# Kernel tuning notes

Hardware: AMD Instinct MI355X
Metric: run time of the kernel (lower is better)

The kernel has to match this reference:

```python
import jax, jax.numpy as jnp
import numpy as np

H = 16   # num_heads
K = 2    # top_k experts per token


def _layer_norm(x, g, b, eps=1e-5):
    mu = jnp.mean(x, axis=-1, keepdims=True)
    var = jnp.mean(jnp.square(x - mu), axis=-1, keepdims=True)
    return (x - mu) * jax.lax.rsqrt(var + eps) * g + b


def setup_inputs() -> dict:
    key = jax.random.key(0)
    ks = jax.random.split(key, 8)
    B, S, D, E = 2, 2048, 1024, 8
    sc = 0.02
    return {
        "x": jax.random.normal(ks[0], (B, S, D), jnp.float32),
        "wq": jax.random.normal(ks[1], (D, D), jnp.float32) * sc,
        "wk": jax.random.normal(ks[2], (D, D), jnp.float32) * sc,
        "wv": jax.random.normal(ks[3], (D, D), jnp.float32) * sc,
        "wo": jax.random.normal(ks[4], (D, D), jnp.float32) * sc,
        "ln1_g": jnp.ones((D,), jnp.float32),
        "ln1_b": jnp.zeros((D,), jnp.float32),
        "ln2_g": jnp.ones((D,), jnp.float32),
        "ln2_b": jnp.zeros((D,), jnp.float32),
        "router_w": jax.random.normal(ks[5], (E, D), jnp.float32) * sc,
        "expert_w": jax.random.normal(ks[6], (E, D, D), jnp.float32) * sc,
    }


def reference(x, wq, wk, wv, wo, ln1_g, ln1_b, ln2_g, ln2_b, router_w, expert_w):
    B, S, D = x.shape
    E = expert_w.shape[0]
    hd = D // H

    # ---- attention sublayer: x = x + attn(norm1(x)) ----
    h = _layer_norm(x, ln1_g, ln1_b)
    q = (h @ wq.T).reshape(B, S, H, hd).transpose(0, 2, 1, 3)  # bhsd
    k = (h @ wk.T).reshape(B, S, H, hd).transpose(0, 2, 1, 3)
    v = (h @ wv.T).reshape(B, S, H, hd).transpose(0, 2, 1, 3)
    scores = jnp.einsum("bhqd,bhkd->bhqk", q, k) / jnp.sqrt(jnp.float32(hd))
    causal = jnp.tril(jnp.ones((S, S), dtype=bool))
    scores = jnp.where(causal, scores, jnp.finfo(scores.dtype).min)
    probs = jax.nn.softmax(scores, axis=-1)
    attn = jnp.einsum("bhqk,bhkd->bhqd", probs, v)
    attn = attn.transpose(0, 2, 1, 3).reshape(B, S, D) @ wo.T
    x = x + attn

    # ---- MoE sublayer: x = x + moe(norm2(x)) ----
    h2 = _layer_norm(x, ln2_g, ln2_b)
    logits = jnp.einsum("bsd,ed->bse", h2, router_w)          # [B,S,E]
    top_logits, top_ids = jax.lax.top_k(logits, K)            # [B,S,K]
    gates = jax.nn.softmax(top_logits, axis=-1)               # [B,S,K]
    # dense combine weights over experts (E is small): sum_k gate_k * onehot(id_k)
    combine = jnp.sum(jax.nn.one_hot(top_ids, E, dtype=h2.dtype) * gates[..., None], axis=-2)  # [B,S,E]
    # per-token matvec with expert weights: token @ W_e.T for each expert, then weighted sum
    y = jnp.einsum("bsd,eod->bseo", h2, expert_w)             # [B,S,E,D]
    moe_out = jnp.einsum("bse,bseo->bso", combine, y)
    return x + moe_out
```

## Files before the change

### kernel.cpp

```cpp
#include <hip/hip_runtime.h>
#include <hip/hip_bf16.h>
#include <cstdint>


typedef __bf16 bf16;
typedef __bf16 bf16x8 __attribute__((ext_vector_type(8)));
typedef __bf16 bf16x4 __attribute__((ext_vector_type(4)));
typedef float f32x4 __attribute__((ext_vector_type(4)));
typedef float f32x16 __attribute__((ext_vector_type(16)));

#define MFMA(a, b, c) __builtin_amdgcn_mfma_f32_16x16x32_bf16(a, b, c, 0, 0, 0)
#define MFMA32(a, b, c) __builtin_amdgcn_mfma_f32_32x32x16_bf16(a, b, c, 0, 0, 0)

__device__ __forceinline__ void gld16(void* lds, const void* g) {
  __builtin_amdgcn_global_load_lds(
      (const __attribute__((address_space(1))) void*)g,
      (__attribute__((address_space(3))) void*)lds, 16, 0, 0);
}

__global__ void prep_weights(const float* __restrict__ wq, const float* __restrict__ wk,
                             const float* __restrict__ wv, const float* __restrict__ wo,
                             const float* __restrict__ expw,
                             bf16* __restrict__ wqh, bf16* __restrict__ wql,
                             bf16* __restrict__ wkh, bf16* __restrict__ wkl,
                             bf16* __restrict__ wvh, bf16* __restrict__ wvl,
                             bf16* __restrict__ woh, bf16* __restrict__ wol,
                             bf16* __restrict__ ewh) {
  int bid = blockIdx.x;
  if (bid < 4096) {
    int wsel = bid >> 10;
    const float* src = wsel == 0 ? wq : wsel == 1 ? wk : wsel == 2 ? wv : wo;
    bf16* hi = wsel == 0 ? wqh : wsel == 1 ? wkh : wsel == 2 ? wvh : woh;
    bf16* lo = wsel == 0 ? wql : wsel == 1 ? wkl : wsel == 2 ? wvl : wol;
    int i = ((bid & 1023) * 256 + threadIdx.x) * 4;
    float4 v = *(const float4*)(src + i);
    float a[4] = {v.x, v.y, v.z, v.w};
#pragma unroll
    for (int j = 0; j < 4; j++) {
      bf16 h = (bf16)a[j];
      hi[i + j] = h;
      lo[i + j] = (bf16)(a[j] - (float)h);
    }
  } else {
    int i = ((bid - 4096) * 256 + threadIdx.x) * 4;
    float4 v = *(const float4*)(expw + i);
    ewh[i] = (bf16)v.x; ewh[i + 1] = (bf16)v.y;
    ewh[i + 2] = (bf16)v.z; ewh[i + 3] = (bf16)v.w;
  }
}

__global__ void ln_split(const float* __restrict__ x, const float* __restrict__ g,
                         const float* __restrict__ b, bf16* __restrict__ hi,
                         bf16* __restrict__ lo) {
  int tok = blockIdx.x, t = threadIdx.x;
  float4 v = ((const float4*)(x + (size_t)tok * 1024))[t];
  float s = v.x + v.y + v.z + v.w;
  float ss = v.x * v.x + v.y * v.y + v.z * v.z + v.w * v.w;
#pragma unroll
  for (int o = 1; o < 64; o <<= 1) { s += __shfl_xor(s, o); ss += __shfl_xor(ss, o); }
  __shared__ float red[8];
  int w = t >> 6, lane = t & 63;
  if (lane == 0) { red[w] = s; red[4 + w] = ss; }
  __syncthreads();
  s = red[0] + red[1] + red[2] + red[3];
  ss = red[4] + red[5] + red[6] + red[7];
  float mu = s * (1.f / 1024.f);
  float rstd = rsqrtf(ss * (1.f / 1024.f) - mu * mu + 1e-5f);
  float4 gv = ((const float4*)g)[t], bv = ((const float4*)b)[t];
  float y[4] = {(v.x - mu) * rstd * gv.x + bv.x, (v.y - mu) * rstd * gv.y + bv.y,
                (v.z - mu) * rstd * gv.z + bv.z, (v.w - mu) * rstd * gv.w + bv.w};
  size_t o = (size_t)tok * 1024 + t * 4;
#pragma unroll
  for (int j = 0; j < 4; j++) {
    bf16 h = (bf16)y[j];
    hi[o + j] = h;
    lo[o + j] = (bf16)(y[j] - (float)h);
  }
}

__global__ void ln2route(const float* __restrict__ x1, const float* __restrict__ g,
                         const float* __restrict__ b, const float* __restrict__ rw,
                         bf16* __restrict__ h2h, int* __restrict__ eid,
                         float2* __restrict__ gout) {
  int tok = blockIdx.x, t = threadIdx.x;
  float4 v = ((const float4*)(x1 + (size_t)tok * 1024))[t];
  float s = v.x + v.y + v.z + v.w;
  float ss = v.x * v.x + v.y * v.y + v.z * v.z + v.w * v.w;
#pragma unroll
  for (int o = 1; o < 64; o <<= 1) { s += __shfl_xor(s, o); ss += __shfl_xor(ss, o); }
  __shared__ float red[8];
  __shared__ float h2s[1024];
  __shared__ float lg[8];
  int w = t >> 6, lane = t & 63;
  if (lane == 0) { red[w] = s; red[4 + w] = ss; }
  __syncthreads();
  s = red[0] + red[1] + red[2] + red[3];
  ss = red[4] + red[5] + red[6] + red[7];
  float mu = s * (1.f / 1024.f);
  float rstd = rsqrtf(ss * (1.f / 1024.f) - mu * mu + 1e-5f);
  float4 gv = ((const float4*)g)[t], bv = ((const float4*)b)[t];
  float4 y;
  y.x = (v.x - mu) * rstd * gv.x + bv.x;
  y.y = (v.y - mu) * rstd * gv.y + bv.y;
  y.z = (v.z - mu) * rstd * gv.z + bv.z;
  y.w = (v.w - mu) * rstd * gv.w + bv.w;
  ((float4*)h2s)[t] = y;
  size_t o = (size_t)tok * 1024 + t * 4;
  h2h[o] = (bf16)y.x; h2h[o + 1] = (bf16)y.y;
  h2h[o + 2] = (bf16)y.z; h2h[o + 3] = (bf16)y.w;
  __syncthreads();
  float a0 = 0.f, a1 = 0.f;
  const float4* r0 = (const float4*)(rw + (2 * w) * 1024);
  const float4* r1 = (const float4*)(rw + (2 * w + 1) * 1024);
#pragma unroll
  for (int it = 0; it < 4; it++) {
    float4 xv = ((const float4*)h2s)[lane + 64 * it];
    float4 w0 = r0[lane + 64 * it];
    float4 w1 = r1[lane + 64 * it];
    a0 += xv.x * w0.x + xv.y * w0.y + xv.z * w0.z + xv.w * w0.w;
    a1 += xv.x * w1.x + xv.y * w1.y + xv.z * w1.z + xv.w * w1.w;
  }
#pragma unroll
  for (int o2 = 1; o2 < 64; o2 <<= 1) {
    a0 += __shfl_xor(a0, o2);
    a1 += __shfl_xor(a1, o2);
  }
  if (lane == 0) { lg[2 * w] = a0; lg[2 * w + 1] = a1; }
  __syncthreads();
  if (t == 0) {
    int i0 = 0; float l0 = lg[0];
#pragma unroll
    for (int e = 1; e < 8; e++) if (lg[e] > l0) { l0 = lg[e]; i0 = e; }
    int i1 = -1; float l1 = -3e38f;
#pragma unroll
    for (int e = 0; e < 8; e++) if (e != i0 && lg[e] > l1) { l1 = lg[e]; i1 = e; }
    float e1 = __expf(l1 - l0);
    float den = 1.f + e1;
    eid[tok] = i0 | (i1 << 4);
    gout[tok] = make_float2(1.f / den, e1 / den);
  }
}

__global__ void build_lists(const int* __restrict__ eid,
                            const float2* __restrict__ gv,
                            int* __restrict__ tlist, float* __restrict__ glist,
                            int* __restrict__ cnt) {
  int e = blockIdx.x, t = threadIdx.x;
  int lane = t & 63, w = t >> 6;
  __shared__ int wt[4];
  int base = 0;
  for (int c = 0; c < 16; c++) {
    int tok = c * 256 + t;
    int pair = eid[tok];
    int e0 = pair & 15, e1 = pair >> 4;
    bool p = (e0 == e) || (e1 == e);
    float2 g2 = gv[tok];
    float gate = (e0 == e) ? g2.x : g2.y;
    unsigned long long m = __ballot(p);
    int rank = __popcll(m & ((1ull << lane) - 1ull));
    if (lane == 0) wt[w] = __popcll(m);
    __syncthreads();
    int off = base;
    for (int i = 0; i < w; i++) off += wt[i];
    if (p) {
      tlist[e * 4096 + off + rank] = tok;
      glist[e * 4096 + off + rank] = gate;
    }
    base += wt[0] + wt[1] + wt[2] + wt[3];
    __syncthreads();
  }
  if (t == 0) cnt[e] = base;
  int pad = (base + 127) & ~127;
  if (pad > 4096) pad = 4096;
  for (int i = base + t; i < pad; i += 256) {
    tlist[e * 4096 + i] = 0;
    glist[e * 4096 + i] = 0.f;
  }
}

__device__ __forceinline__ void gemm_core_split(
    const bf16* __restrict__ Ah, const bf16* __restrict__ Al,
    const bf16* __restrict__ Bh, const bf16* __restrict__ Bl, int m0, int n0,
    f32x4 (&acc)[4][4]) {
  __shared__ __align__(16) bf16 As_h[4096], As_l[4096], Bs_h[4096], Bs_l[4096];
  int t = threadIdx.x, lane = t & 63, w = t >> 6;
  int i0 = t, i1 = t + 256;
  const bf16* a0h = Ah + (size_t)(m0 + (i0 >> 2)) * 1024 + (i0 & 3) * 8;
  const bf16* a1h = Ah + (size_t)(m0 + (i1 >> 2)) * 1024 + (i1 & 3) * 8;
  const bf16* a0l = Al + (size_t)(m0 + (i0 >> 2)) * 1024 + (i0 & 3) * 8;
  const bf16* a1l = Al + (size_t)(m0 + (i1 >> 2)) * 1024 + (i1 & 3) * 8;
  const bf16* b0h = Bh + (size_t)(n0 + (i0 >> 2)) * 1024 + (i0 & 3) * 8;
  const bf16* b1h = Bh + (size_t)(n0 + (i1 >> 2)) * 1024 + (i1 & 3) * 8;
  const bf16* b0l = Bl + (size_t)(n0 + (i0 >> 2)) * 1024 + (i0 & 3) * 8;
  const bf16* b1l = Bl + (size_t)(n0 + (i1 >> 2)) * 1024 + (i1 & 3) * 8;
  int wm = (w >> 1) * 64, wn = (w & 1) * 64;
  int lr = lane & 15, lq = lane >> 4;
  for (int k0 = 0; k0 < 1024; k0 += 32) {
    __syncthreads();
    gld16(&As_h[i0 * 8], a0h + k0); gld16(&As_h[i1 * 8], a1h + k0);
    gld16(&As_l[i0 * 8], a0l + k0); gld16(&As_l[i1 * 8], a1l + k0);
    gld16(&Bs_h[i0 * 8], b0h + k0); gld16(&Bs_h[i1 * 8], b1h + k0);
    gld16(&Bs_l[i0 * 8], b0l + k0); gld16(&Bs_l[i1 * 8], b1l + k0);
    __syncthreads();
    bf16x8 ah[4], al4[4], bh[4], bl4[4];
#pragma unroll
    for (int i = 0; i < 4; i++) {
      ah[i]  = *(const bf16x8*)&As_h[(wm + i * 16 + lr) * 32 + lq * 8];
      al4[i] = *(const bf16x8*)&As_l[(wm + i * 16 + lr) * 32 + lq * 8];
      bh[i]  = *(const bf16x8*)&Bs_h[(wn + i * 16 + lr) * 32 + lq * 8];
      bl4[i] = *(const bf16x8*)&Bs_l[(wn + i * 16 + lr) * 32 + lq * 8];
    }
#pragma unroll
    for (int i = 0; i < 4; i++)
#pragma unroll
      for (int j = 0; j < 4; j++) {
        f32x4 c = acc[i][j];
        c = MFMA(ah[i], bh[j], c);
        c = MFMA(ah[i], bl4[j], c);
        c = MFMA(al4[i], bh[j], c);
        acc[i][j] = c;
      }
  }
}

__global__ __launch_bounds__(256, 2) void gemm_qk(
    const bf16* __restrict__ hh, const bf16* __restrict__ hl,
    const bf16* __restrict__ wqh, const bf16* __restrict__ wql,
    const bf16* __restrict__ wkh, const bf16* __restrict__ wkl,
    bf16* __restrict__ qh, bf16* __restrict__ ql, bf16* __restrict__ kh,
    bf16* __restrict__ kl) {
  int n0 = blockIdx.x * 128, m0 = blockIdx.y * 128, z = blockIdx.z;
  const bf16* Bh = z ? wkh : wqh;
  const bf16* Bl = z ? wkl : wql;
  f32x4 acc[4][4];
#pragma unroll
  for (int i = 0; i < 4; i++)
#pragma unroll
    for (int j = 0; j < 4; j++) acc[i][j] = (f32x4){0.f, 0.f, 0.f, 0.f};
  gemm_core_split(hh, hl, Bh, Bl, m0, n0, acc);
  int t = threadIdx.x, lane = t & 63, w = t >> 6;
  int wm = (w >> 1) * 64, wn = (w & 1) * 64, lr = lane & 15, lq = lane >> 4;
  bf16* Oh = z ? kh : qh;
  bf16* Ol = z ? kl : ql;
  float scale = z ? 1.0f : (0.125f * 1.44269504f);
#pragma unroll
  for (int i = 0; i < 4; i++)
#pragma unroll
    for (int j = 0; j < 4; j++)
#pragma unroll
      for (int r = 0; r < 4; r++) {
        size_t row = m0 + wm + i * 16 + lq * 4 + r;
        int col = n0 + wn + j * 16 + lr;
        float v = acc[i][j][r] * scale;
        bf16 h = (bf16)v;
        Oh[row * 1024 + col] = h;
        Ol[row * 1024 + col] = (bf16)(v - (float)h);
      }
}

__global__ __launch_bounds__(256, 2) void gemm_v(
    const bf16* __restrict__ A, const bf16* __restrict__ B,
    bf16* __restrict__ vth) {
  int n0 = blockIdx.x * 128, m0 = blockIdx.y * 128;
  __shared__ __align__(16) bf16 As[4096], Bs[4096];
  int t = threadIdx.x, lane = t & 63, w = t >> 6;
  int i0 = t, i1 = t + 256;
  const bf16* a0 = A + (size_t)(m0 + (i0 >> 2)) * 1024 + (i0 & 3) * 8;
  const bf16* a1 = A + (size_t)(m0 + (i1 >> 2)) * 1024 + (i1 & 3) * 8;
  const bf16* b0 = B + (size_t)(n0 + (i0 >> 2)) * 1024 + (i0 & 3) * 8;
  const bf16* b1 = B + (size_t)(n0 + (i1 >> 2)) * 1024 + (i1 & 3) * 8;
  int wm = (w >> 1) * 64, wn = (w & 1) * 64, lr = lane & 15, lq = lane >> 4;
  f32x4 acc[4][4];
#pragma unroll
  for (int i = 0; i < 4; i++)
#pragma unroll
    for (int j = 0; j < 4; j++) acc[i][j] = (f32x4){0.f, 0.f, 0.f, 0.f};
  for (int k0 = 0; k0 < 1024; k0 += 32) {
    __syncthreads();
    gld16(&As[i0 * 8], a0 + k0); gld16(&As[i1 * 8], a1 + k0);
    gld16(&Bs[i0 * 8], b0 + k0); gld16(&Bs[i1 * 8], b1 + k0);
    __syncthreads();
    bf16x8 af[4], bfr[4];
#pragma unroll
    for (int i = 0; i < 4; i++) {
      af[i] = *(const bf16x8*)&As[(wm + i * 16 + lr) * 32 + lq * 8];
      bfr[i] = *(const bf16x8*)&Bs[(wn + i * 16 + lr) * 32 + lq * 8];
    }
#pragma unroll
    for (int i = 0; i < 4; i++)
#pragma unroll
      for (int j = 0; j < 4; j++) acc[i][j] = MFMA(af[i], bfr[j], acc[i][j]);
  }
  int bb = m0 >> 11;
  int srow0 = m0 & 2047;
#pragma unroll
  for (int i = 0; i < 4; i++)
#pragma unroll
    for (int j = 0; j < 4; j++) {
      int col = n0 + wn + j * 16 + lr;
      int head = col >> 6, d = col & 63;
      int s = srow0 + wm + i * 16 + lq * 4;
      int ss = (s & ~63) | (((((s >> 2) & 15)) ^ (d & 15)) << 2);
      bf16x4 hv;
#pragma unroll
      for (int r = 0; r < 4; r++) hv[r] = (bf16)acc[i][j][r];
      size_t off = ((size_t)((bb * 16 + head) * 64 + d)) * 2048 + ss;
      *(bf16x4*)(vth + off) = hv;
    }
}

__global__ __launch_bounds__(256, 2) void gemm_wo(
    const bf16* __restrict__ ah, const bf16* __restrict__ al,
    const bf16* __restrict__ bh, const bf16* __restrict__ bl,
    const float* __restrict__ resid, float* __restrict__ outp) {
  int n0 = blockIdx.x * 128, m0 = blockIdx.y * 128;
  f32x4 acc[4][4];
#pragma unroll
  for (int i = 0; i < 4; i++)
#pragma unroll
    for (int j = 0; j < 4; j++) acc[i][j] = (f32x4){0.f, 0.f, 0.f, 0.f};
  gemm_core_split(ah, al, bh, bl, m0, n0, acc);
  int t = threadIdx.x, lane = t & 63, w = t >> 6;
  int wm = (w >> 1) * 64, wn = (w & 1) * 64, lr = lane & 15, lq = lane >> 4;
#pragma unroll
  for (int i = 0; i < 4; i++)
#pragma unroll
    for (int j = 0; j < 4; j++)
#pragma unroll
      for (int r = 0; r < 4; r++) {
        size_t row = m0 + wm + i * 16 + lq * 4 + r;
        int col = n0 + wn + j * 16 + lr;
        outp[row * 1024 + col] = resid[row * 1024 + col] + acc[i][j][r];
      }
}

__global__ __launch_bounds__(256, 3) void attn_fused(
    const bf16* __restrict__ qh, const bf16* __restrict__ ql,
    const bf16* __restrict__ kh, const bf16* __restrict__ kl,
    const bf16* __restrict__ vth,
    float* __restrict__ O_acc, float* __restrict__ L_acc) {
  const int S = 2048, D = 1024;
  static const unsigned char QTt[40] = {
      15, 15, 15, 15, 14, 14, 14, 13, 13, 13, 12, 12, 12, 11, 11, 11,
      10, 10, 9, 9, 8, 8, 7, 7, 6, 5, 4, 3,
      14, 10, 6, 2, 13, 9, 5, 1, 12, 8, 4, 0};
  static const unsigned char C0t[40] = {
      0, 8, 16, 24, 0, 8, 16, 0, 8, 16, 0, 8, 16, 0, 8, 16,
      0, 8, 0, 8, 0, 8, 0, 8, 0, 0, 0, 0,
      24, 16, 8, 0, 24, 16, 8, 0, 24, 16, 8, 0};
  static const unsigned char C1t[40] = {
      8, 16, 24, 32, 8, 16, 24, 8, 16, 24, 8, 16, 24, 8, 16, 24,
      8, 16, 8, 16, 8, 16, 8, 16, 8, 8, 8, 8,
      30, 22, 14, 6, 28, 20, 12, 4, 26, 18, 10, 2};
  int y = blockIdx.y;
  int qt = QTt[y];
  int tile0 = C0t[y], tile1 = C1t[y];
  int hb = blockIdx.x;
  int head = hb & 15, b = hb >> 4;
  int qb = qt * 128;
  int t = threadIdx.x, lane = t & 63, w = t >> 6;
  int l31 = lane & 31, l5 = lane >> 5;
  int base = b * S, hcol = head * 64;

  __shared__ __align__(16) bf16 Kh_s[2][4096], Kl_s[2][4096];
  __shared__ __align__(16) bf16 Vh_s[2][4096];

  bf16x8 qfh[4], qfl[4];
  {
    const bf16* p1 = qh + (size_t)(base + qb + w * 32 + l31) * D + hcol + l5 * 8;
    const bf16* p2 = ql + (size_t)(base + qb + w * 32 + l31) * D + hcol + l5 * 8;
#pragma unroll
    for (int c = 0; c < 4; c++) {
      qfh[c] = *(const bf16x8*)(p1 + 16 * c);
      qfl[c] = *(const bf16x8*)(p2 + 16 * c);
    }
  }
  f32x16 O0, O1;
  float lsum = 0.f;
#pragma unroll
  for (int r = 0; r < 16; r++) { O0[r] = 0.f; O1[r] = 0.f; }

  int r0 = t >> 3, p0 = t & 7;
  int g0 = p0 ^ (r0 & 7);
  const bf16* k0hp = kh + (size_t)(base + r0) * D + hcol + g0 * 8;
  const bf16* k1hp = kh + (size_t)(base + 32 + r0) * D + hcol + g0 * 8;
  const bf16* k0lp = kl + (size_t)(base + r0) * D + hcol + g0 * 8;
  const bf16* k1lp = kl + (size_t)(base + 32 + r0) * D + hcol + g0 * 8;
  const bf16* v0hp = vth + (size_t)(hb * 64 + r0) * 2048 + p0 * 8;
  const bf16* v1hp = vth + (size_t)(hb * 64 + 32 + r0) * 2048 + p0 * 8;

  int qwmin = qb + w * 32;

#define STAGE(kts, bb) do { \
    gld16(&Kh_s[bb][t * 8], k0hp + (size_t)(kts) * D); \
    gld16(&Kh_s[bb][2048 + t * 8], k1hp + (size_t)(kts) * D); \
    gld16(&Kl_s[bb][t * 8], k0lp + (size_t)(kts) * D); \
    gld16(&Kl_s[bb][2048 + t * 8], k1lp + (size_t)(kts) * D); \
    gld16(&Vh_s[bb][t * 8], v0hp + (kts)); \
    gld16(&Vh_s[bb][2048 + t * 8], v1hp + (kts)); \
  } while (0)

  STAGE(tile0 * 64, tile0 & 1);
  __syncthreads();

  for (int ti = tile0; ti < tile1; ++ti) {
    int kt = ti * 64;
    int bb = ti & 1;
    if (ti + 1 < tile1) STAGE((ti + 1) * 64, bb ^ 1);
    if (kt <= qwmin + 31) {
      bool skip1 = (kt + 32 > qwmin + 31);
#pragma unroll
      for (int ktile = 0; ktile < 2; ktile++) {
        if (ktile == 1 && skip1) break;
        bool maskt = (kt + 32 * ktile + 31 > qwmin);
        int keyr = ktile * 32 + l31;
        f32x16 scA, scB;
#pragma unroll
        for (int r = 0; r < 16; r++) { scA[r] = 0.f; scB[r] = 0.f; }
        __builtin_amdgcn_s_setprio(1);
#pragma unroll
        for (int c = 0; c < 4; c++) {
          int dg = ((2 * c + l5) ^ (keyr & 7)) * 8;
          bf16x8 kv = *(const bf16x8*)&Kh_s[bb][keyr * 64 + dg];
          bf16x8 km = *(const bf16x8*)&Kl_s[bb][keyr * 64 + dg];
          if (c < 2) {
            scA = MFMA32(kv, qfh[c], scA);
            scA = MFMA32(kv, qfl[c], scA);
            scA = MFMA32(km, qfh[c], scA);
          } else {
            scB = MFMA32(kv, qfh[c], scB);
            scB = MFMA32(kv, qfl[c], scB);
            scB = MFMA32(km, qfh[c], scB);
          }
        }
        __builtin_amdgcn_s_setprio(0);
        int kb0 = kt + 32 * ktile + 4 * l5;
        int qg = qwmin + l31;
        float pvv[16];
#pragma unroll
        for (int r = 0; r < 16; r++) {
          int cst = (r & 3) + 8 * (r >> 2);
          float sv = scA[r] + scB[r];
          if (maskt && (kb0 + cst > qg)) sv = -30000.f;
          float p = __builtin_amdgcn_exp2f(sv);
          pvv[r] = p;
          lsum += p;
        }
        uint32_t hw[4][2], lw[4][2];
#pragma unroll
        for (int o = 0; o < 4; o++)
#pragma unroll
          for (int j = 0; j < 2; j++) {
            int ra = 4 * o + 2 * j;
            bf16 h0 = (bf16)pvv[ra], h1 = (bf16)pvv[ra + 1];
            union { bf16 h[2]; uint32_t u; } ph, pl;
            ph.h[0] = h0; ph.h[1] = h1;
            pl.h[0] = (bf16)(pvv[ra] - (float)h0);
            pl.h[1] = (bf16)(pvv[ra + 1] - (float)h1);
            hw[o][j] = ph.u;
            lw[o][j] = pl.u;
          }
#pragma unroll
        for (int c2 = 0; c2 < 2; c2++) {
          union { uint32_t u[4]; bf16x8 v; } pa, plo;
          pa.u[0] = hw[2 * c2][0];     pa.u[1] = hw[2 * c2][1];
          pa.u[2] = hw[2 * c2 + 1][0]; pa.u[3] = hw[2 * c2 + 1][1];
          plo.u[0] = lw[2 * c2][0];     plo.u[1] = lw[2 * c2][1];
          plo.u[2] = lw[2 * c2 + 1][0]; plo.u[3] = lw[2 * c2 + 1][1];
          __builtin_amdgcn_s_setprio(1);
#pragma unroll
          for (int dtile = 0; dtile < 2; dtile++) {
            int d = dtile * 32 + l31;
            int pqA = ((8 * ktile + 4 * c2 + l5) ^ (d & 15)) * 4;
            union { bf16x4 q[2]; bf16x8 v; } vbu;
            vbu.q[0] = *(const bf16x4*)&Vh_s[bb][d * 64 + pqA];
            vbu.q[1] = *(const bf16x4*)&Vh_s[bb][d * 64 + (pqA ^ 8)];
            if (dtile == 0) {
              O0 = MFMA32(pa.v, vbu.v, O0);
              O0 = MFMA32(plo.v, vbu.v, O0);
            } else {
              O1 = MFMA32(pa.v, vbu.v, O1);
              O1 = MFMA32(plo.v, vbu.v, O1);
            }
          }
          __builtin_amdgcn_s_setprio(0);
        }
      }
    }
    __syncthreads();
  }
#undef STAGE
  if (tile0 * 64 <= qwmin + 31) {
    float ltot = lsum + __shfl_xor(lsum, 32);
    if (l5 == 0) {
      size_t tokq = (size_t)(base + qb + w * 32 + l31);
      atomicAdd(&L_acc[tokq * 16 + head], ltot);
    }
#pragma unroll
    for (int r = 0; r < 16; r++) {
      int qlocal = (r & 3) + 8 * (r >> 2) + 4 * l5;
      size_t tok = (size_t)(base + qb + w * 32 + qlocal);
      atomicAdd(&O_acc[tok * 1024 + hcol + l31], O0[r]);
      atomicAdd(&O_acc[tok * 1024 + hcol + 32 + l31], O1[r]);
    }
  }
}

__global__ void attn_final(const float* __restrict__ O_acc,
                           const float* __restrict__ L_acc,
                           bf16* __restrict__ oh, bf16* __restrict__ ol) {
  int tok = blockIdx.x, t = threadIdx.x;
  float4 v = ((const float4*)(O_acc + (size_t)tok * 1024))[t];
  float linv = 1.f / L_acc[tok * 16 + (t >> 4)];
  float a[4] = {v.x * linv, v.y * linv, v.z * linv, v.w * linv};
  bf16x4 hv, lv;
#pragma unroll
  for (int j = 0; j < 4; j++) {
    bf16 h = (bf16)a[j];
    hv[j] = h;
    lv[j] = (bf16)(a[j] - (float)h);
  }
  size_t o = (size_t)tok * 1024 + t * 4;
  *(bf16x4*)(oh + o) = hv;
  *(bf16x4*)(ol + o) = lv;
}

__global__ __launch_bounds__(256, 2) void gemm_moe(
    const bf16* __restrict__ A, const bf16* __restrict__ W,
    const int* __restrict__ tlist, const float* __restrict__ glist,
    const int* __restrict__ cnt, float* __restrict__ outp) {
  int e = blockIdx.z;
  int count = cnt[e];
  int m0 = blockIdx.y * 128;
  if (m0 >= count) return;
  int n0 = blockIdx.x * 128;
  const int* tl = tlist + e * 4096;
  const bf16* B = W + (size_t)e * 1024 * 1024;
  __shared__ __align__(16) bf16 As[4096], Bs[4096];
  int t = threadIdx.x, lane = t & 63, w = t >> 6;
  int i0 = t, i1 = t + 256;
  int ra = tl[m0 + (i0 >> 2)], rb = tl[m0 + (i1 >> 2)];
  const bf16* a0 = A + (size_t)ra * 1024 + (i0 & 3) * 8;
  const bf16* a1 = A + (size_t)rb * 1024 + (i1 & 3) * 8;
  const bf16* b0 = B + (size_t)(n0 + (i0 >> 2)) * 1024 + (i0 & 3) * 8;
  const bf16* b1 = B + (size_t)(n0 + (i1 >> 2)) * 1024 + (i1 & 3) * 8;
  int wm = (w >> 1) * 64, wn = (w & 1) * 64, lr = lane & 15, lq = lane >> 4;
  f32x4 acc[4][4];
#pragma unroll
  for (int i = 0; i < 4; i++)
#pragma unroll
    for (int j = 0; j < 4; j++) acc[i][j] = (f32x4){0.f, 0.f, 0.f, 0.f};
  for (int k0 = 0; k0 < 1024; k0 += 32) {
    __syncthreads();
    gld16(&As[i0 * 8], a0 + k0); gld16(&As[i1 * 8], a1 + k0);
    gld16(&Bs[i0 * 8], b0 + k0); gld16(&Bs[i1 * 8], b1 + k0);
    __syncthreads();
    bf16x8 af[4], bfr[4];
#pragma unroll
    for (int i = 0; i < 4; i++) {
      af[i] = *(const bf16x8*)&As[(wm + i * 16 + lr) * 32 + lq * 8];
      bfr[i] = *(const bf16x8*)&Bs[(wn + i * 16 + lr) * 32 + lq * 8];
    }
#pragma unroll
    for (int i = 0; i < 4; i++)
#pragma unroll
      for (int j = 0; j < 4; j++) acc[i][j] = MFMA(af[i], bfr[j], acc[i][j]);
  }
#pragma unroll
  for (int i = 0; i < 4; i++)
#pragma unroll
    for (int r = 0; r < 4; r++) {
      int slot = m0 + wm + i * 16 + lq * 4 + r;
      if (slot < count) {
        int tok = tl[slot];
        float gte = glist[e * 4096 + slot];
#pragma unroll
        for (int j = 0; j < 4; j++) {
          int col = n0 + wn + j * 16 + lr;
          atomicAdd(&outp[(size_t)tok * 1024 + col], gte * acc[i][j][r]);
        }
      }
    }
}

extern "C" void kernel_launch(void* const* d_in, const int* in_sizes, int n_in,
                              void* d_out, int out_size, void* d_ws, size_t ws_size,
                              hipStream_t stream) {
  (void)in_sizes; (void)n_in; (void)out_size; (void)ws_size;
  const float* x    = (const float*)d_in[0];
  const float* wq   = (const float*)d_in[1];
  const float* wk   = (const float*)d_in[2];
  const float* wv   = (const float*)d_in[3];
  const float* wo   = (const float*)d_in[4];
  const float* ln1g = (const float*)d_in[5];
  const float* ln1b = (const float*)d_in[6];
  const float* ln2g = (const float*)d_in[7];
  const float* ln2b = (const float*)d_in[8];
  const float* rw   = (const float*)d_in[9];
  const float* expw = (const float*)d_in[10];
  float* out = (float*)d_out;

  char* p = (char*)d_ws;
  auto take = [&](size_t bytes) -> char* {
    char* r = p;
    p += (bytes + 255) & ~(size_t)255;
    return r;
  };
  const size_t ND2 = 4096ull * 1024 * 2;
  const size_t WD2 = 1024ull * 1024 * 2;
  bf16* h_hi = (bf16*)take(ND2); bf16* h_lo = (bf16*)take(ND2);
  bf16* wqh = (bf16*)take(WD2); bf16* wql = (bf16*)take(WD2);
  bf16* wkh = (bf16*)take(WD2); bf16* wkl = (bf16*)take(WD2);
  bf16* wvh = (bf16*)take(WD2); bf16* wvl = (bf16*)take(WD2);
  bf16* woh = (bf16*)take(WD2); bf16* wol = (bf16*)take(WD2);
  bf16* q_hi = (bf16*)take(ND2); bf16* q_lo = (bf16*)take(ND2);
  bf16* k_hi = (bf16*)take(ND2); bf16* k_lo = (bf16*)take(ND2);
  bf16* vt_hi = (bf16*)take(ND2);
  bf16* a_hi = (bf16*)take(ND2); bf16* a_lo = (bf16*)take(ND2);
  bf16* h2h  = (bf16*)take(ND2);
  bf16* ewh  = (bf16*)take(8ull * 1024 * 1024 * 2);
  int*   tlist  = (int*)take(8ull * 4096 * 4);
  float* glist  = (float*)take(8ull * 4096 * 4);
  int*   cnt    = (int*)take(64);
  int*   reid   = (int*)take(4096 * 4);
  float2* rg    = (float2*)take(4096 * 8);
  float* O_acc  = (float*)take(4096ull * 1024 * 4);
  float* L_acc  = (float*)take(4096ull * 16 * 4);

  hipMemsetAsync(O_acc, 0, 4096ull * 1024 * 4, stream);
  hipMemsetAsync(L_acc, 0, 4096ull * 16 * 4, stream);
  prep_weights<<<12288, 256, 0, stream>>>(wq, wk, wv, wo, expw, wqh, wql, wkh,
                                          wkl, wvh, wvl, woh, wol, ewh);
  ln_split<<<4096, 256, 0, stream>>>(x, ln1g, ln1b, h_hi, h_lo);
  gemm_qk<<<dim3(8, 32, 2), 256, 0, stream>>>(h_hi, h_lo, wqh, wql, wkh, wkl,
                                              q_hi, q_lo, k_hi, k_lo);
  gemm_v<<<dim3(8, 32), 256, 0, stream>>>(h_hi, wvh, vt_hi);
  attn_fused<<<dim3(32, 40), 256, 0, stream>>>(q_hi, q_lo, k_hi, k_lo, vt_hi,
                                               O_acc, L_acc);
  attn_final<<<4096, 256, 0, stream>>>(O_acc, L_acc, a_hi, a_lo);
  gemm_wo<<<dim3(8, 32), 256, 0, stream>>>(a_hi, a_lo, woh, wol, x, out);
  ln2route<<<4096, 256, 0, stream>>>(out, ln2g, ln2b, rw, h2h, reid, rg);
  build_lists<<<8, 256, 0, stream>>>(reid, rg, tlist, glist, cnt);
  gemm_moe<<<dim3(8, 32, 8), 256, 0, stream>>>(h2h, ewh, tlist, glist, cnt,
                                               out);
}
```

Measured before the change: 418.9 us.

## Fuse attention normalization into Wo GEMM, add unmasked attention fast path, drop unused wv lo

Removes the attn_final kernel: gemm_wo now reads the fp32 O_acc/L_acc directly, normalizes by 1/L, and splits into hi/lo bf16 while staging the A tile into LDS. This avoids writing and re-reading two bf16 activation buffers. The attention loop is split into helper functions and gains a fast path for fully unmasked 64-key tiles that computes both QK subtiles back to back without mask checks. prep_weights also stops producing the unused Wv low-part buffer. The fused GEMM's A loads are now synchronous register loads with conversion work inside the K loop, which may reduce overlap compared with the previous core.

```diff
diff --git a/kernel.cpp b/kernel.cpp
--- a/kernel.cpp
+++ b/kernel.cpp
@@ -23,7 +23,7 @@
                              const float* __restrict__ expw,
                              bf16* __restrict__ wqh, bf16* __restrict__ wql,
                              bf16* __restrict__ wkh, bf16* __restrict__ wkl,
-                             bf16* __restrict__ wvh, bf16* __restrict__ wvl,
+                             bf16* __restrict__ wvh,
                              bf16* __restrict__ woh, bf16* __restrict__ wol,
                              bf16* __restrict__ ewh) {
   int bid = blockIdx.x;
@@ -31,7 +31,7 @@
     int wsel = bid >> 10;
     const float* src = wsel == 0 ? wq : wsel == 1 ? wk : wsel == 2 ? wv : wo;
     bf16* hi = wsel == 0 ? wqh : wsel == 1 ? wkh : wsel == 2 ? wvh : woh;
-    bf16* lo = wsel == 0 ? wql : wsel == 1 ? wkl : wsel == 2 ? wvl : wol;
+    bf16* lo = wsel == 0 ? wql : wsel == 1 ? wkl : wsel == 2 ? (bf16*)nullptr : wol;
     int i = ((bid & 1023) * 256 + threadIdx.x) * 4;
     float4 v = *(const float4*)(src + i);
     float a[4] = {v.x, v.y, v.z, v.w};
@@ -39,7 +39,7 @@
     for (int j = 0; j < 4; j++) {
       bf16 h = (bf16)a[j];
       hi[i + j] = h;
-      lo[i + j] = (bf16)(a[j] - (float)h);
+      if (wsel != 2) lo[i + j] = (bf16)(a[j] - (float)h);
     }
   } else {
     int i = ((bid - 4096) * 256 + threadIdx.x) * 4;
@@ -310,18 +310,72 @@
 }
 
 __global__ __launch_bounds__(256, 2) void gemm_wo(
-    const bf16* __restrict__ ah, const bf16* __restrict__ al,
+    const float* __restrict__ Oacc, const float* __restrict__ Lacc,
     const bf16* __restrict__ bh, const bf16* __restrict__ bl,
     const float* __restrict__ resid, float* __restrict__ outp) {
   int n0 = blockIdx.x * 128, m0 = blockIdx.y * 128;
+  __shared__ __align__(16) bf16 As_h[4096], As_l[4096], Bs_h[4096], Bs_l[4096];
+  int t = threadIdx.x, lane = t & 63, w = t >> 6;
+  int i0 = t, i1 = t + 256;
+  int row0 = m0 + (i0 >> 2), row1 = m0 + (i1 >> 2);
+  const float* a0 = Oacc + (size_t)row0 * 1024 + (i0 & 3) * 8;
+  const float* a1 = Oacc + (size_t)row1 * 1024 + (i1 & 3) * 8;
+  const bf16* b0h = bh + (size_t)(n0 + (i0 >> 2)) * 1024 + (i0 & 3) * 8;
+  const bf16* b1h = bh + (size_t)(n0 + (i1 >> 2)) * 1024 + (i1 & 3) * 8;
+  const bf16* b0l = bl + (size_t)(n0 + (i0 >> 2)) * 1024 + (i0 & 3) * 8;
+  const bf16* b1l = bl + (size_t)(n0 + (i1 >> 2)) * 1024 + (i1 & 3) * 8;
+  int wm = (w >> 1) * 64, wn = (w & 1) * 64;
+  int lr = lane & 15, lq = lane >> 4;
   f32x4 acc[4][4];
 #pragma unroll
   for (int i = 0; i < 4; i++)
 #pragma unroll
     for (int j = 0; j < 4; j++) acc[i][j] = (f32x4){0.f, 0.f, 0.f, 0.f};
-  gemm_core_split(ah, al, bh, bl, m0, n0, acc);
-  int t = threadIdx.x, lane = t & 63, w = t >> 6;
-  int wm = (w >> 1) * 64, wn = (w & 1) * 64, lr = lane & 15, lq = lane >> 4;
+  for (int k0 = 0; k0 < 1024; k0 += 32) {
+    __syncthreads();
+    gld16(&Bs_h[i0 * 8], b0h + k0); gld16(&Bs_h[i1 * 8], b1h + k0);
+    gld16(&Bs_l[i0 * 8], b0l + k0); gld16(&Bs_l[i1 * 8], b1l + k0);
+    int hd = k0 >> 6;
+    float linv0 = 1.f / Lacc[row0 * 16 + hd];
+    float linv1 = 1.f / Lacc[row1 * 16 + hd];
+    float4 va0 = *(const float4*)(a0 + k0);
+    float4 vb0 = *(const float4*)(a0 + k0 + 4);
+    float4 va1 = *(const float4*)(a1 + k0);
+    float4 vb1 = *(const float4*)(a1 + k0 + 4);
+    float f0[8] = {va0.x, va0.y, va0.z, va0.w, vb0.x, vb0.y, vb0.z, vb0.w};
+    float f1[8] = {va1.x, va1.y, va1.z, va1.w, vb1.x, vb1.y, vb1.z, vb1.w};
+    bf16x8 h0, l0, h1, l1;
+#pragma unroll
+    for (int j = 0; j < 8; j++) {
+      float x0 = f0[j] * linv0;
+      bf16 hh0 = (bf16)x0;
+      h0[j] = hh0; l0[j] = (bf16)(x0 - (float)hh0);
+      float x1 = f1[j] * linv1;
+      bf16 hh1 = (bf16)x1;
+      h1[j] = hh1; l1[j] = (bf16)(x1 - (float)hh1);
+    }
+    *(bf16x8*)&As_h[i0 * 8] = h0; *(bf16x8*)&As_l[i0 * 8] = l0;
+    *(bf16x8*)&As_h[i1 * 8] = h1; *(bf16x8*)&As_l[i1 * 8] = l1;
+    __syncthreads();
+    bf16x8 ah[4], al4[4], bhf[4], bl4[4];
+#pragma unroll
+    for (int i = 0; i < 4; i++) {
+      ah[i]  = *(const bf16x8*)&As_h[(wm + i * 16 + lr) * 32 + lq * 8];
+      al4[i] = *(const bf16x8*)&As_l[(wm + i * 16 + lr) * 32 + lq * 8];
+      bhf[i] = *(const bf16x8*)&Bs_h[(wn + i * 16 + lr) * 32 + lq * 8];
+      bl4[i] = *(const bf16x8*)&Bs_l[(wn + i * 16 + lr) * 32 + lq * 8];
+    }
+#pragma unroll
+    for (int i = 0; i < 4; i++)
+#pragma unroll
+      for (int j = 0; j < 4; j++) {
+        f32x4 c = acc[i][j];
+        c = MFMA(ah[i], bhf[j], c);
+        c = MFMA(ah[i], bl4[j], c);
+        c = MFMA(al4[i], bhf[j], c);
+        acc[i][j] = c;
+      }
+  }
 #pragma unroll
   for (int i = 0; i < 4; i++)
 #pragma unroll
@@ -332,6 +386,85 @@
         int col = n0 + wn + j * 16 + lr;
         outp[row * 1024 + col] = resid[row * 1024 + col] + acc[i][j][r];
       }
+}
+
+__device__ __forceinline__ f32x16 qk_subtile(
+    const bf16* __restrict__ Ks, const bf16* __restrict__ Kls, int keyr, int l5,
+    const bf16x8 (&qfh)[4], const bf16x8 (&qfl)[4]) {
+  f32x16 sA, sB;
+#pragma unroll
+  for (int r = 0; r < 16; r++) { sA[r] = 0.f; sB[r] = 0.f; }
+#pragma unroll
+  for (int c = 0; c < 4; c++) {
+    int dg = ((2 * c + l5) ^ (keyr & 7)) * 8;
+    bf16x8 kv = *(const bf16x8*)&Ks[keyr * 64 + dg];
+    bf16x8 km = *(const bf16x8*)&Kls[keyr * 64 + dg];
+    if (c < 2) {
+      sA = MFMA32(kv, qfh[c], sA);
+      sA = MFMA32(kv, qfl[c], sA);
+      sA = MFMA32(km, qfh[c], sA);
+    } else {
+      sB = MFMA32(kv, qfh[c], sB);
+      sB = MFMA32(kv, qfl[c], sB);
+      sB = MFMA32(km, qfh[c], sB);
+    }
+  }
+  return sA + sB;
+}
+
+__device__ __forceinline__ void exp_pack_pv(
+    f32x16 sc, bool maskt, int kb0, int qg, int ktile,
+    float& lsum, f32x16& O0, f32x16& O1,
+    const bf16* __restrict__ Vs, int l31, int l5) {
+  float pvv[16];
+#pragma unroll
+  for (int r = 0; r < 16; r++) {
+    int cst = (r & 3) + 8 * (r >> 2);
+    float sv = sc[r];
+    if (maskt && (kb0 + cst > qg)) sv = -30000.f;
+    float p = __builtin_amdgcn_exp2f(sv);
+    pvv[r] = p;
+    lsum += p;
+  }
+  uint32_t hw[4][2], lw[4][2];
+#pragma unroll
+  for (int o = 0; o < 4; o++)
+#pragma unroll
+    for (int j = 0; j < 2; j++) {
+      int ra = 4 * o + 2 * j;
+      bf16 h0 = (bf16)pvv[ra], h1 = (bf16)pvv[ra + 1];
+      union { bf16 h[2]; uint32_t u; } ph, pl;
+      ph.h[0] = h0; ph.h[1] = h1;
+      pl.h[0] = (bf16)(pvv[ra] - (float)h0);
+      pl.h[1] = (bf16)(pvv[ra + 1] - (float)h1);
+      hw[o][j] = ph.u;
+      lw[o][j] = pl.u;
+    }
+#pragma unroll
+  for (int c2 = 0; c2 < 2; c2++) {
+    union { uint32_t u[4]; bf16x8 v; } pa, plo;
+    pa.u[0] = hw[2 * c2][0];     pa.u[1] = hw[2 * c2][1];
+    pa.u[2] = hw[2 * c2 + 1][0]; pa.u[3] = hw[2 * c2 + 1][1];
+    plo.u[0] = lw[2 * c2][0];     plo.u[1] = lw[2 * c2][1];
+    plo.u[2] = lw[2 * c2 + 1][0]; plo.u[3] = lw[2 * c2 + 1][1];
+    __builtin_amdgcn_s_setprio(1);
+#pragma unroll
+    for (int dtile = 0; dtile < 2; dtile++) {
+      int d = dtile * 32 + l31;
+      int pqA = ((8 * ktile + 4 * c2 + l5) ^ (d & 15)) * 4;
+      union { bf16x4 q[2]; bf16x8 v; } vbu;
+      vbu.q[0] = *(const bf16x4*)&Vs[d * 64 + pqA];
+      vbu.q[1] = *(const bf16x4*)&Vs[d * 64 + (pqA ^ 8)];
+      if (dtile == 0) {
+        O0 = MFMA32(pa.v, vbu.v, O0);
+        O0 = MFMA32(plo.v, vbu.v, O0);
+      } else {
+        O1 = MFMA32(pa.v, vbu.v, O1);
+        O1 = MFMA32(plo.v, vbu.v, O1);
+      }
+    }
+    __builtin_amdgcn_s_setprio(0);
+  }
 }
 
 __global__ __launch_bounds__(256, 3) void attn_fused(
@@ -407,84 +540,28 @@
     int kt = ti * 64;
     int bb = ti & 1;
     if (ti + 1 < tile1) STAGE((ti + 1) * 64, bb ^ 1);
-    if (kt <= qwmin + 31) {
+    const bf16* Ks = &Kh_s[bb][0];
+    const bf16* Kls = &Kl_s[bb][0];
+    const bf16* Vs = &Vh_s[bb][0];
+    if (kt + 64 <= qb) {
+      __builtin_amdgcn_s_setprio(1);
+      f32x16 sc0 = qk_subtile(Ks, Kls, l31, l5, qfh, qfl);
+      f32x16 sc1 = qk_subtile(Ks, Kls, 32 + l31, l5, qfh, qfl);
+      __builtin_amdgcn_s_setprio(0);
+      exp_pack_pv(sc0, false, 0, 0, 0, lsum, O0, O1, Vs, l31, l5);
+      exp_pack_pv(sc1, false, 0, 0, 1, lsum, O0, O1, Vs, l31, l5);
+    } else if (kt <= qwmin + 31) {
       bool skip1 = (kt + 32 > qwmin + 31);
 #pragma unroll
       for (int ktile = 0; ktile < 2; ktile++) {
         if (ktile == 1 && skip1) break;
         bool maskt = (kt + 32 * ktile + 31 > qwmin);
-        int keyr = ktile * 32 + l31;
-        f32x16 scA, scB;
-#pragma unroll
-        for (int r = 0; r < 16; r++) { scA[r] = 0.f; scB[r] = 0.f; }
         __builtin_amdgcn_s_setprio(1);
-#pragma unroll
-        for (int c = 0; c < 4; c++) {
-          int dg = ((2 * c + l5) ^ (keyr & 7)) * 8;
-          bf16x8 kv = *(const bf16x8*)&Kh_s[bb][keyr * 64 + dg];
-          bf16x8 km = *(const bf16x8*)&Kl_s[bb][keyr * 64 + dg];
-          if (c < 2) {
-            scA = MFMA32(kv, qfh[c], scA);
-            scA = MFMA32(kv, qfl[c], scA);
-            scA = MFMA32(km, qfh[c], scA);
-          } else {
-            scB = MFMA32(kv, qfh[c], scB);
-            scB = MFMA32(kv, qfl[c], scB);
-            scB = MFMA32(km, qfh[c], scB);
-          }
-        }
+        f32x16 sc = qk_subtile(Ks, Kls, ktile * 32 + l31, l5, qfh, qfl);
         __builtin_amdgcn_s_setprio(0);
         int kb0 = kt + 32 * ktile + 4 * l5;
         int qg = qwmin + l31;
-        float pvv[16];
-#pragma unroll
-        for (int r = 0; r < 16; r++) {
-          int cst = (r & 3) + 8 * (r >> 2);
-          float sv = scA[r] + scB[r];
-          if (maskt && (kb0 + cst > qg)) sv = -30000.f;
-          float p = __builtin_amdgcn_exp2f(sv);
-          pvv[r] = p;
-          lsum += p;
-        }
-        uint32_t hw[4][2], lw[4][2];
-#pragma unroll
-        for (int o = 0; o < 4; o++)
-#pragma unroll
-          for (int j = 0; j < 2; j++) {
-            int ra = 4 * o + 2 * j;
-            bf16 h0 = (bf16)pvv[ra], h1 = (bf16)pvv[ra + 1];
-            union { bf16 h[2]; uint32_t u; } ph, pl;
-            ph.h[0] = h0; ph.h[1] = h1;
-            pl.h[0] = (bf16)(pvv[ra] - (float)h0);
-            pl.h[1] = (bf16)(pvv[ra + 1] - (float)h1);
-            hw[o][j] = ph.u;
-            lw[o][j] = pl.u;
-          }
-#pragma unroll
-        for (int c2 = 0; c2 < 2; c2++) {
-          union { uint32_t u[4]; bf16x8 v; } pa, plo;
-          pa.u[0] = hw[2 * c2][0];     pa.u[1] = hw[2 * c2][1];
-          pa.u[2] = hw[2 * c2 + 1][0]; pa.u[3] = hw[2 * c2 + 1][1];
-          plo.u[0] = lw[2 * c2][0];     plo.u[1] = lw[2 * c2][1];
-          plo.u[2] = lw[2 * c2 + 1][0]; plo.u[3] = lw[2 * c2 + 1][1];
-          __builtin_amdgcn_s_setprio(1);
-#pragma unroll
-          for (int dtile = 0; dtile < 2; dtile++) {
-            int d = dtile * 32 + l31;
-            int pqA = ((8 * ktile + 4 * c2 + l5) ^ (d & 15)) * 4;
-            union { bf16x4 q[2]; bf16x8 v; } vbu;
-            vbu.q[0] = *(const bf16x4*)&Vh_s[bb][d * 64 + pqA];
-            vbu.q[1] = *(const bf16x4*)&Vh_s[bb][d * 64 + (pqA ^ 8)];
-            if (dtile == 0) {
-              O0 = MFMA32(pa.v, vbu.v, O0);
-              O0 = MFMA32(plo.v, vbu.v, O0);
-            } else {
-              O1 = MFMA32(pa.v, vbu.v, O1);
-              O1 = MFMA32(plo.v, vbu.v, O1);
-            }
-          }
-          __builtin_amdgcn_s_setprio(0);
-        }
+        exp_pack_pv(sc, maskt, kb0, qg, ktile, lsum, O0, O1, Vs, l31, l5);
       }
     }
     __syncthreads();
@@ -504,25 +581,6 @@
       atomicAdd(&O_acc[tok * 1024 + hcol + 32 + l31], O1[r]);
     }
   }
-}
-
-__global__ void attn_final(const float* __restrict__ O_acc,
-                           const float* __restrict__ L_acc,
-                           bf16* __restrict__ oh, bf16* __restrict__ ol) {
-  int tok = blockIdx.x, t = threadIdx.x;
-  float4 v = ((const float4*)(O_acc + (size_t)tok * 1024))[t];
-  float linv = 1.f / L_acc[tok * 16 + (t >> 4)];
-  float a[4] = {v.x * linv, v.y * linv, v.z * linv, v.w * linv};
-  bf16x4 hv, lv;
-#pragma unroll
-  for (int j = 0; j < 4; j++) {
-    bf16 h = (bf16)a[j];
-    hv[j] = h;
-    lv[j] = (bf16)(a[j] - (float)h);
-  }
-  size_t o = (size_t)tok * 1024 + t * 4;
-  *(bf16x4*)(oh + o) = hv;
-  *(bf16x4*)(ol + o) = lv;
 }
 
 __global__ __launch_bounds__(256, 2) void gemm_moe(
@@ -611,12 +669,11 @@
   bf16* h_hi = (bf16*)take(ND2); bf16* h_lo = (bf16*)take(ND2);
   bf16* wqh = (bf16*)take(WD2); bf16* wql = (bf16*)take(WD2);
   bf16* wkh = (bf16*)take(WD2); bf16* wkl = (bf16*)take(WD2);
-  bf16* wvh = (bf16*)take(WD2); bf16* wvl = (bf16*)take(WD2);
+  bf16* wvh = (bf16*)take(WD2);
   bf16* woh = (bf16*)take(WD2); bf16* wol = (bf16*)take(WD2);
   bf16* q_hi = (bf16*)take(ND2); bf16* q_lo = (bf16*)take(ND2);
   bf16* k_hi = (bf16*)take(ND2); bf16* k_lo = (bf16*)take(ND2);
   bf16* vt_hi = (bf16*)take(ND2);
-  bf16* a_hi = (bf16*)take(ND2); bf16* a_lo = (bf16*)take(ND2);
   bf16* h2h  = (bf16*)take(ND2);
   bf16* ewh  = (bf16*)take(8ull * 1024 * 1024 * 2);
   int*   tlist  = (int*)take(8ull * 4096 * 4);
@@ -630,15 +687,14 @@
   hipMemsetAsync(O_acc, 0, 4096ull * 1024 * 4, stream);
   hipMemsetAsync(L_acc, 0, 4096ull * 16 * 4, stream);
   prep_weights<<<12288, 256, 0, stream>>>(wq, wk, wv, wo, expw, wqh, wql, wkh,
-                                          wkl, wvh, wvl, woh, wol, ewh);
+                                          wkl, wvh, woh, wol, ewh);
   ln_split<<<4096, 256, 0, stream>>>(x, ln1g, ln1b, h_hi, h_lo);
   gemm_qk<<<dim3(8, 32, 2), 256, 0, stream>>>(h_hi, h_lo, wqh, wql, wkh, wkl,
                                               q_hi, q_lo, k_hi, k_lo);
   gemm_v<<<dim3(8, 32), 256, 0, stream>>>(h_hi, wvh, vt_hi);
   attn_fused<<<dim3(32, 40), 256, 0, stream>>>(q_hi, q_lo, k_hi, k_lo, vt_hi,
                                                O_acc, L_acc);
-  attn_final<<<4096, 256, 0, stream>>>(O_acc, L_acc, a_hi, a_lo);
-  gemm_wo<<<dim3(8, 32), 256, 0, stream>>>(a_hi, a_lo, woh, wol, x, out);
+  gemm_wo<<<dim3(8, 32), 256, 0, stream>>>(O_acc, L_acc, woh, wol, x, out);
   ln2route<<<4096, 256, 0, stream>>>(out, ln2g, ln2b, rw, h2h, reid, rg);
   build_lists<<<8, 256, 0, stream>>>(reid, rg, tlist, glist, cnt);
   gemm_moe<<<dim3(8, 32, 8), 256, 0, stream>>>(h2h, ewh, tlist, glist, cnt,
```

Measured after the change: 415.0 us. Within noise of the previous version (-0.9%).
